# Kernel optimization log

Hardware: AMD Instinct MI355X
Metric: run time of the kernel (lower is better)

Reference implementation:

```python
import jax, jax.numpy as jnp
import numpy as np

INPUT_DIM = 1024
HIDDEN_DIM = 1024


def setup_inputs() -> dict:
    key = jax.random.key(0)
    ks = jax.random.split(key, 7)
    s = 1.0 / np.sqrt(INPUT_DIM)
    x = jax.random.normal(ks[0], (4, 2048, INPUT_DIM), dtype=jnp.float32)
    Wq = jax.random.uniform(ks[1], (INPUT_DIM, HIDDEN_DIM), minval=-s, maxval=s, dtype=jnp.float32)
    bq = jax.random.uniform(ks[2], (HIDDEN_DIM,), minval=-s, maxval=s, dtype=jnp.float32)
    Wk = jax.random.uniform(ks[3], (INPUT_DIM, HIDDEN_DIM), minval=-s, maxval=s, dtype=jnp.float32)
    bk = jax.random.uniform(ks[4], (HIDDEN_DIM,), minval=-s, maxval=s, dtype=jnp.float32)
    Wv = jax.random.uniform(ks[5], (INPUT_DIM, HIDDEN_DIM), minval=-s, maxval=s, dtype=jnp.float32)
    bv = jax.random.uniform(ks[6], (HIDDEN_DIM,), minval=-s, maxval=s, dtype=jnp.float32)
    return {"x": x, "Wq": Wq, "bq": bq, "Wk": Wk, "bk": bk, "Wv": Wv, "bv": bv}


def reference(x, Wq, bq, Wk, bk, Wv, bv):
    # Q, K, V: [B, S, H]
    Q = jnp.einsum('bsd,dh->bsh', x, Wq) + bq
    K = jnp.einsum('bsd,dh->bsh', x, Wk) + bk
    V = jnp.einsum('bsd,dh->bsh', x, Wv) + bv
    scale = 1.0 / jnp.sqrt(jnp.array(Q.shape[-1], dtype=Q.dtype))
    scores = jnp.einsum('bqh,bkh->bqk', Q, K) * scale  # [B, S, S]
    attn = jax.nn.softmax(scores, axis=-1)
    return jnp.einsum('bqk,bkh->bqh', attn, V)
```

## Files before the change

kernel.cpp:

```cpp
#include <hip/hip_runtime.h>
#include <hip/hip_bf16.h>
#include <stdint.h>

typedef unsigned short u16;
typedef __attribute__((ext_vector_type(8))) short short8;
typedef __attribute__((ext_vector_type(4))) float floatx4;

#define DIM 1024

__device__ inline u16 f2bf(float f) {
  union { float f; uint32_t u; } v; v.f = f;
  uint32_t r = v.u + 0x7fffu + ((v.u >> 16) & 1u);
  return (u16)(r >> 16);
}

__device__ inline uint32_t f2bf2(float lo, float hi) {
  __hip_bfloat162 h = __float22bfloat162_rn(float2{lo, hi});
  union { __hip_bfloat162 h; uint32_t u; } v; v.h = h;
  return v.u;
}

__device__ inline void gload_lds16(const u16* g, u16* l) {
  __builtin_amdgcn_global_load_lds((const __attribute__((address_space(1))) uint32_t*)g,
                                   (__attribute__((address_space(3))) uint32_t*)l,
                                   16, 0, 0);
}

#define LGKM0 asm volatile("s_waitcnt lgkmcnt(0)" ::: "memory")
#define VMW(n) asm volatile("s_waitcnt vmcnt(" #n ")" ::: "memory")
#define BAR() do { asm volatile("" ::: "memory"); __builtin_amdgcn_s_barrier(); asm volatile("" ::: "memory"); } while (0)
#define PRIO1 __builtin_amdgcn_s_setprio(1)
#define PRIO0 __builtin_amdgcn_s_setprio(0)

__global__ __launch_bounds__(256) void prep(const float* __restrict__ x,
                                            const float* __restrict__ Wq,
                                            const float* __restrict__ Wk,
                                            const float* __restrict__ Wv,
                                            const float* __restrict__ bq,
                                            const float* __restrict__ bk,
                                            const float* __restrict__ bv,
                                            u16* __restrict__ Xb,
                                            u16* __restrict__ Wt,
                                            float* __restrict__ bias,
                                            float* __restrict__ lsum) {
  __shared__ u16 tile[32][33];
  const int bx = blockIdx.x;
  if (bx < 8192) {
    size_t i = ((size_t)bx * 256 + threadIdx.x) * 4;
    float4 v = *(const float4*)(x + i);
    uint2 o;
    o.x = f2bf2(v.x, v.y);
    o.y = f2bf2(v.z, v.w);
    *(uint2*)(Xb + i) = o;
    if (bx < 8) {
      float4 z = {0.f, 0.f, 0.f, 0.f};
      *(float4*)(lsum + (size_t)bx * 1024 + threadIdx.x * 4) = z;
    }
    return;
  }
  const int t = bx - 8192;
  const int tz = t >> 10;
  const int bxx = t & 31;
  const int byy = (t >> 5) & 31;
  const float* W = (tz == 0) ? Wq : (tz == 1) ? Wk : Wv;
  u16* o = Wt + (size_t)tz * (1u << 20);
  if (bxx == 0 && byy == 0) {
    const float* bsrc = (tz == 0) ? bq : (tz == 1) ? bk : bv;
    float4 b4 = *(const float4*)(bsrc + threadIdx.x * 4);
    *(float4*)(bias + tz * 1024 + threadIdx.x * 4) = b4;
  }
  int c0 = bxx * 32, r0 = byy * 32;
  int tx = threadIdx.x & 31, ty = threadIdx.x >> 5;
#pragma unroll
  for (int p = 0; p < 4; ++p)
    tile[p * 8 + ty][tx] = f2bf(W[(size_t)(r0 + p * 8 + ty) * DIM + c0 + tx]);
  __syncthreads();
#pragma unroll
  for (int p = 0; p < 4; ++p)
    o[(size_t)(c0 + p * 8 + ty) * DIM + r0 + tx] = tile[tx][p * 8 + ty];
}

__device__ __forceinline__ void gemm1024_8ph(const u16* __restrict__ Ab,
                                             const u16* __restrict__ Bb,
                                             u16* __restrict__ lds,
                                             floatx4 (&acc)[8][4]) {
  constexpr int K = 1024;
  constexpr int BUF = 32768;
  const int tid = threadIdx.x;
  const int lane = tid & 63;
  const int w = tid >> 6;
  const int wm = (w >> 2) * 128;
  const int wn = (w & 3) * 64;
  const int fr = lane & 15;
  const int sl0 = (((lane >> 4)    ) ^ (fr & 7)) * 8;
  const int sl1 = (((lane >> 4) | 4) ^ (fr & 7)) * 8;
  const int rA = (wm + fr) * 64;
  const int rB = 16384 + (wn + fr) * 64;
  const int srow = tid >> 3;
  const int kc = ((tid & 7) ^ (srow & 7)) * 8;
  const u16* ga = Ab + (size_t)srow * K + kc;
  const u16* gb = Bb + (size_t)srow * K + kc;
  u16* const ld0 = lds + w * 512;

  short8 Aq[4][2], Bp[2][2][2];

#define STG_A(B_, TT, h) { u16* d_ = ld0 + (B_) * BUF + (h) * 8192;               \
    const u16* s_ = ga + (size_t)((h) * 128) * K + (TT) * 64;                     \
    gload_lds16(s_, d_); gload_lds16(s_ + (size_t)64 * K, d_ + 4096); }
#define STG_B(B_, TT, h) { u16* d_ = ld0 + (B_) * BUF + 16384 + (h) * 8192;       \
    const u16* s_ = gb + (size_t)((h) * 128) * K + (TT) * 64;                     \
    gload_lds16(s_, d_); gload_lds16(s_ + (size_t)64 * K, d_ + 4096); }
#define RD_A(B_, q) { const u16* p_ = lds + (B_) * BUF + rA + (q) * 4096;         \
    _Pragma("unroll") for (int m_ = 0; m_ < 4; ++m_) {                            \
      Aq[m_][0] = *(const short8*)(p_ + m_ * 1024 + sl0);                         \
      Aq[m_][1] = *(const short8*)(p_ + m_ * 1024 + sl1); } }
#define RD_B(B_, p) { const u16* q_ = lds + (B_) * BUF + rB + (p) * 2048;         \
    _Pragma("unroll") for (int n_ = 0; n_ < 2; ++n_) {                            \
      Bp[p][n_][0] = *(const short8*)(q_ + n_ * 1024 + sl0);                      \
      Bp[p][n_][1] = *(const short8*)(q_ + n_ * 1024 + sl1); } }
#define MM(q, p)                                                                  \
    _Pragma("unroll") for (int m_ = 0; m_ < 4; ++m_)                              \
    _Pragma("unroll") for (int n_ = 0; n_ < 2; ++n_)                              \
    _Pragma("unroll") for (int s_ = 0; s_ < 2; ++s_)                              \
      acc[(q) * 4 + m_][(p) * 2 + n_] = __builtin_amdgcn_mfma_f32_16x16x32_bf16(  \
          Aq[m_][s_], Bp[p][n_][s_], acc[(q) * 4 + m_][(p) * 2 + n_], 0, 0, 0);

  STG_A(0, 0, 0); STG_A(0, 0, 1); STG_B(0, 0, 0); STG_B(0, 0, 1);
  STG_B(1, 1, 0); STG_B(1, 1, 1);
  VMW(4);
  BAR();

  for (int j = 0; j < 8; ++j) {
    const int T = 2 * j;
    const bool nl = (j < 7);
    RD_A(0, 0); RD_B(0, 0);
    STG_A(1, T + 1, 0);
    BAR(); LGKM0;
    PRIO1; MM(0, 0); PRIO0;
    BAR();
    RD_B(0, 1);
    STG_A(1, T + 1, 1);
    BAR(); LGKM0;
    PRIO1; MM(0, 1); PRIO0;
    BAR();
    RD_A(0, 1);
    if (nl) STG_B(0, T + 2, 0);
    BAR(); LGKM0;
    PRIO1; MM(1, 0); PRIO0;
    BAR();
    if (nl) STG_B(0, T + 2, 1);
    BAR(); LGKM0;
    PRIO1; MM(1, 1); PRIO0;
    if (nl) { VMW(4); } else { VMW(0); }
    BAR();
    RD_A(1, 0); RD_B(1, 0);
    if (nl) STG_A(0, T + 2, 0);
    BAR(); LGKM0;
    PRIO1; MM(0, 0); PRIO0;
    BAR();
    RD_B(1, 1);
    if (nl) STG_A(0, T + 2, 1);
    BAR(); LGKM0;
    PRIO1; MM(0, 1); PRIO0;
    BAR();
    RD_A(1, 1);
    if (nl) STG_B(1, T + 3, 0);
    BAR(); LGKM0;
    PRIO1; MM(1, 0); PRIO0;
    BAR();
    if (nl) STG_B(1, T + 3, 1);
    BAR(); LGKM0;
    PRIO1; MM(1, 1); PRIO0;
    if (nl) { VMW(4); } else { VMW(0); }
    BAR();
  }
#undef STG_A
#undef STG_B
#undef RD_A
#undef RD_B
#undef MM
}

__global__ __launch_bounds__(512, 2)
void qk_proj(const u16* __restrict__ Xb, const u16* __restrict__ Wt,
             u16* __restrict__ Q, const float* __restrict__ bias) {
  __shared__ __align__(16) u16 lds[65536];
  const int x = blockIdx.x;
  const int c = x & 7, j = x >> 3;
  const int mt = c * 4 + (j & 3);
  const int nt = j >> 2;
  const u16* Ab = Xb + (size_t)mt * 262144;
  const u16* Bb = Wt + (size_t)nt * 262144;
  floatx4 acc[8][4] = {};
  gemm1024_8ph(Ab, Bb, lds, acc);

  const int lane = threadIdx.x & 63;
  const int w = threadIdx.x >> 6;
  const int wm = (w >> 2) * 128, wn = (w & 3) * 64;
  const int er = (lane >> 4) * 4, ec = lane & 15;
  const int r0 = mt * 256 + wm;
  const int z = nt >> 2;
  const int c0 = (nt & 3) * 256 + wn;
  u16* C = Q + (size_t)z * (8u << 20);
  const float* bz = bias + z * 1024;
  const float zs = (z == 0) ? 0.03125f : 1.0f;
#pragma unroll
  for (int mi = 0; mi < 8; ++mi)
#pragma unroll
    for (int ni = 0; ni < 4; ++ni) {
      const int col = c0 + ni * 16 + ec;
      const float bb = bz[col];
      const int row = r0 + mi * 16 + er;
      const uint32_t p0 = f2bf2((acc[mi][ni][0] + bb) * zs, (acc[mi][ni][1] + bb) * zs);
      const uint32_t p1 = f2bf2((acc[mi][ni][2] + bb) * zs, (acc[mi][ni][3] + bb) * zs);
      C[(size_t)(row + 0) * 1024 + col] = (u16)p0;
      C[(size_t)(row + 1) * 1024 + col] = (u16)(p0 >> 16);
      C[(size_t)(row + 2) * 1024 + col] = (u16)p1;
      C[(size_t)(row + 3) * 1024 + col] = (u16)(p1 >> 16);
    }
}

__global__ __launch_bounds__(512, 2)
void vt_score(const u16* __restrict__ Xb, const u16* __restrict__ Wt,
              const u16* __restrict__ Q, u16* __restrict__ Vt,
              u16* __restrict__ P, float* __restrict__ lsum,
              const float* __restrict__ bias) {
  __shared__ __align__(16) u16 lds[65536];
  const int x = blockIdx.x;
  const u16 *Ab, *Bb;
  int mt, nt, z = 0;
  if (x < 128) {
    mt = x & 3; nt = x >> 2;
    Ab = Wt + (size_t)2 * (1u << 20) + (size_t)mt * 262144;
    Bb = Xb + (size_t)nt * 262144;
  } else {
    const int xs = x - 128;
    z = xs >> 6;
    const int q = xs & 63;
    const int c = q & 7, jj = q >> 3;
    mt = (c & 3) * 2 + (jj & 1);
    nt = (c >> 2) * 4 + (jj >> 1);
    Ab = Q + (size_t)z * 2097152 + (size_t)mt * 262144;
    Bb = Q + 8388608 + (size_t)z * 2097152 + (size_t)nt * 262144;
  }
  floatx4 acc[8][4] = {};
  gemm1024_8ph(Ab, Bb, lds, acc);

  const int lane = threadIdx.x & 63;
  const int w = threadIdx.x >> 6;
  const int wm = (w >> 2) * 128, wn = (w & 3) * 64;
  const int er = (lane >> 4) * 4, ec = lane & 15;
  const int r0 = mt * 256 + wm;
  const int c0 = nt * 256 + wn;

  if (x < 128) {
    const float* bz = bias + 2 * 1024;
#pragma unroll
    for (int mi = 0; mi < 8; ++mi) {
      float bb[4];
#pragma unroll
      for (int r = 0; r < 4; ++r) bb[r] = bz[r0 + mi * 16 + er + r];
#pragma unroll
      for (int ni = 0; ni < 4; ++ni) {
        const int col = c0 + ni * 16 + ec;
        const size_t base = (size_t)(col >> 11) * (1u << 21) + (col & 2047);
        const int row = r0 + mi * 16 + er;
        const uint32_t p0 = f2bf2(acc[mi][ni][0] + bb[0], acc[mi][ni][1] + bb[1]);
        const uint32_t p1 = f2bf2(acc[mi][ni][2] + bb[2], acc[mi][ni][3] + bb[3]);
        Vt[base + (size_t)(row + 0) * 2048] = (u16)p0;
        Vt[base + (size_t)(row + 1) * 2048] = (u16)(p0 >> 16);
        Vt[base + (size_t)(row + 2) * 2048] = (u16)p1;
        Vt[base + (size_t)(row + 3) * 2048] = (u16)(p1 >> 16);
      }
    }
  } else {
    u16* C = P + (size_t)z * (4u << 20);
    float* lz = lsum + z * 2048;
#pragma unroll
    for (int mi = 0; mi < 8; ++mi) {
      float rs[4] = {0.f, 0.f, 0.f, 0.f};
#pragma unroll
      for (int ni = 0; ni < 4; ++ni) {
        const int col = c0 + ni * 16 + ec;
        const int row = r0 + mi * 16 + er;
        float e[4];
#pragma unroll
        for (int r = 0; r < 4; ++r) {
          e[r] = exp2f(acc[mi][ni][r] * 1.44269504088896340736f);
          rs[r] += e[r];
        }
        const uint32_t p0 = f2bf2(e[0], e[1]);
        const uint32_t p1 = f2bf2(e[2], e[3]);
        C[(size_t)(row + 0) * 2048 + col] = (u16)p0;
        C[(size_t)(row + 1) * 2048 + col] = (u16)(p0 >> 16);
        C[(size_t)(row + 2) * 2048 + col] = (u16)p1;
        C[(size_t)(row + 3) * 2048 + col] = (u16)(p1 >> 16);
      }
#pragma unroll
      for (int o = 1; o < 16; o <<= 1)
#pragma unroll
        for (int r = 0; r < 4; ++r) rs[r] += __shfl_xor(rs[r], o);
      if ((lane & 15) == 0) {
#pragma unroll
        for (int r = 0; r < 4; ++r)
          atomicAdd(&lz[r0 + mi * 16 + er + r], rs[r]);
      }
    }
  }
}

__global__ __launch_bounds__(512, 2)
void pv_out(const u16* __restrict__ P, const u16* __restrict__ Vt,
            float* __restrict__ out, const float* __restrict__ lsum) {
  __shared__ __align__(16) u16 lds[49152];
  constexpr int K = 2048;
  constexpr int BUF = 24576;
  const int x = blockIdx.x;
  const int z = x >> 6, q = x & 63;
  const int c = q & 7, jj = q >> 3;
  const int mt = (c >> 1) * 4 + (jj & 3);
  const int nt = (c & 1) * 2 + (jj >> 2);
  const u16* Ab = P + (size_t)z * (4u << 20) + (size_t)mt * 128 * 2048;
  const u16* Bb = Vt + (size_t)z * (2u << 20) + (size_t)nt * 256 * 2048;

  const int tid = threadIdx.x;
  const int lane = tid & 63;
  const int w = tid >> 6;
  const int wm = (w >> 2) * 64;
  const int wn = (w & 3) * 64;
  const int fr = lane & 15;
  const int sl0 = (((lane >> 4)    ) ^ (fr & 7)) * 8;
  const int sl1 = (((lane >> 4) | 4) ^ (fr & 7)) * 8;
  const int rA = (wm + fr) * 64;
  const int rB = 8192 + (wn + fr) * 64;
  const int srow = tid >> 3;
  const int kc = ((tid & 7) ^ (srow & 7)) * 8;
  const u16* ga = Ab + (size_t)srow * K + kc;
  const u16* gb = Bb + (size_t)srow * K + kc;
  u16* const ld0 = lds + w * 512;

  short8 Aq[4][2], Bp[2][2][2];
  floatx4 acc[4][4] = {};

#define PSTG_A(B_, TT) { u16* d_ = ld0 + (B_) * BUF;                              \
    const u16* s_ = ga + (size_t)(TT) * 64;                                       \
    gload_lds16(s_, d_); gload_lds16(s_ + (size_t)64 * K, d_ + 4096); }
#define PSTG_B(B_, TT, h) { u16* d_ = ld0 + (B_) * BUF + 8192 + (h) * 8192;       \
    const u16* s_ = gb + (size_t)((h) * 128) * K + (TT) * 64;                     \
    gload_lds16(s_, d_); gload_lds16(s_ + (size_t)64 * K, d_ + 4096); }
#define PRD_A(B_) { const u16* p_ = lds + (B_) * BUF + rA;                        \
    _Pragma("unroll") for (int m_ = 0; m_ < 4; ++m_) {                            \
      Aq[m_][0] = *(const short8*)(p_ + m_ * 1024 + sl0);                         \
      Aq[m_][1] = *(const short8*)(p_ + m_ * 1024 + sl1); } }
#define PRD_B(B_, p) { const u16* q_ = lds + (B_) * BUF + rB + (p) * 2048;        \
    _Pragma("unroll") for (int n_ = 0; n_ < 2; ++n_) {                            \
      Bp[p][n_][0] = *(const short8*)(q_ + n_ * 1024 + sl0);                      \
      Bp[p][n_][1] = *(const short8*)(q_ + n_ * 1024 + sl1); } }
#define PMM(p)                                                                    \
    _Pragma("unroll") for (int m_ = 0; m_ < 4; ++m_)                              \
    _Pragma("unroll") for (int n_ = 0; n_ < 2; ++n_)                              \
    _Pragma("unroll") for (int s_ = 0; s_ < 2; ++s_)                              \
      acc[m_][(p) * 2 + n_] = __builtin_amdgcn_mfma_f32_16x16x32_bf16(            \
          Aq[m_][s_], Bp[p][n_][s_], acc[m_][(p) * 2 + n_], 0, 0, 0);

  PSTG_A(0, 0); PSTG_B(0, 0, 0); PSTG_B(0, 0, 1); PSTG_A(1, 1);
  VMW(2);
  BAR();

  for (int j = 0; j < 16; ++j) {
    const int T = 2 * j;
    const bool nl = (j < 15);
    PRD_A(0); PRD_B(0, 0);
    PSTG_B(1, T + 1, 0); PSTG_B(1, T + 1, 1);
    BAR(); LGKM0;
    PRIO1; PMM(0); PRIO0;
    BAR();
    PRD_B(0, 1);
    if (nl) PSTG_A(0, T + 2);
    BAR(); LGKM0;
    PRIO1; PMM(1); PRIO0;
    if (nl) { VMW(2); } else { VMW(0); }
    BAR();
    PRD_A(1); PRD_B(1, 0);
    if (nl) { PSTG_B(0, T + 2, 0); PSTG_B(0, T + 2, 1); }
    BAR(); LGKM0;
    PRIO1; PMM(0); PRIO0;
    BAR();
    PRD_B(1, 1);
    if (nl) PSTG_A(1, T + 3);
    BAR(); LGKM0;
    PRIO1; PMM(1); PRIO0;
    if (nl) { VMW(2); } else { VMW(0); }
    BAR();
  }
#undef PSTG_A
#undef PSTG_B
#undef PRD_A
#undef PRD_B
#undef PMM

  const int er = (lane >> 4) * 4, ec = lane & 15;
  const int r0 = mt * 128 + wm;
  const int c0 = nt * 256 + wn;
  float* C = out + (size_t)z * (2048 * 1024);
  const float* lz = lsum + z * 2048;
#pragma unroll
  for (int mi = 0; mi < 4; ++mi) {
    float inv[4];
#pragma unroll
    for (int r = 0; r < 4; ++r) inv[r] = 1.0f / lz[r0 + mi * 16 + er + r];
#pragma unroll
    for (int ni = 0; ni < 4; ++ni) {
      const int col = c0 + ni * 16 + ec;
#pragma unroll
      for (int r = 0; r < 4; ++r)
        C[(size_t)(r0 + mi * 16 + er + r) * 1024 + col] = acc[mi][ni][r] * inv[r];
    }
  }
}

extern "C" void kernel_launch(void* const* d_in, const int* in_sizes, int n_in,
                              void* d_out, int out_size, void* d_ws, size_t ws_size,
                              hipStream_t stream) {
  const float* x  = (const float*)d_in[0];
  const float* Wq = (const float*)d_in[1];
  const float* bq = (const float*)d_in[2];
  const float* Wk = (const float*)d_in[3];
  const float* bk = (const float*)d_in[4];
  const float* Wv = (const float*)d_in[5];
  const float* bv = (const float*)d_in[6];
  float* out = (float*)d_out;

  char* ws = (char*)d_ws;
  const size_t MB = 1ull << 20;
  u16* Q    = (u16*)(ws + 0 * MB);
  u16* Vt   = (u16*)(ws + 48 * MB);
  u16* Xb   = (u16*)(ws + 64 * MB);
  u16* Wt   = (u16*)(ws + 80 * MB);
  float* bias = (float*)(ws + 86 * MB);
  float* lsum = (float*)(ws + 87 * MB);
  u16* P    = (u16*)(ws + 88 * MB);
  (void)ws_size; (void)in_sizes; (void)n_in; (void)out_size;

  prep<<<11264, 256, 0, stream>>>(x, Wq, Wk, Wv, bq, bk, bv, Xb, Wt, bias, lsum);
  qk_proj<<<256, 512, 0, stream>>>(Xb, Wt, Q, bias);
  vt_score<<<384, 512, 0, stream>>>(Xb, Wt, Q, Vt, P, lsum, bias);
  pv_out<<<256, 512, 0, stream>>>(P, Vt, out, lsum);
}
```

Measured before the change: 234.3 us.

## Restructure GEMM pipelines to prefetch two k-tiles ahead into the buffer just consumed

```diff
diff --git a/kernel.cpp b/kernel.cpp
--- a/kernel.cpp
+++ b/kernel.cpp
@@ -80,11 +80,12 @@
     o[(size_t)(c0 + p * 8 + ty) * DIM + r0 + tx] = tile[tx][p * 8 + ty];
 }
 
-__device__ __forceinline__ void gemm1024_8ph(const u16* __restrict__ Ab,
+__device__ __forceinline__ void gemm1024_4ph(const u16* __restrict__ Ab,
                                              const u16* __restrict__ Bb,
                                              u16* __restrict__ lds,
                                              floatx4 (&acc)[8][4]) {
   constexpr int K = 1024;
+  constexpr int NT = 16;
   constexpr int BUF = 32768;
   const int tid = threadIdx.x;
   const int lane = tid & 63;
@@ -125,60 +126,49 @@
       acc[(q) * 4 + m_][(p) * 2 + n_] = __builtin_amdgcn_mfma_f32_16x16x32_bf16(  \
           Aq[m_][s_], Bp[p][n_][s_], acc[(q) * 4 + m_][(p) * 2 + n_], 0, 0, 0);
 
+#define HALF_ITER(U)                                                              \
+  {                                                                               \
+    const int u_ = (U) & 1;                                                       \
+    const bool st_ = (U) + 2 < NT;                                                \
+                                                                          \
+    RD_B(u_, 0); RD_B(u_, 1); RD_A(u_, 0);                                        \
+    BAR(); LGKM0;                                                                 \
+    PRIO1; MM(0, 0); PRIO0;                                                       \
+    BAR();                                                                        \
+                                                                          \
+    if (st_) STG_B(u_, (U) + 2, 0);                                               \
+    BAR(); LGKM0;                                                                 \
+    PRIO1; MM(0, 1); PRIO0;                                                       \
+    BAR();                                                                        \
+                                                                          \
+    RD_A(u_, 1);                                                                  \
+    if (st_) STG_B(u_, (U) + 2, 1);                                               \
+    BAR(); LGKM0;                                                                 \
+    PRIO1; MM(1, 0); PRIO0;                                                       \
+    BAR();                                                                        \
+                                                                          \
+    if (st_) { STG_A(u_, (U) + 2, 0); STG_A(u_, (U) + 2, 1); }                    \
+    BAR(); LGKM0;                                                                 \
+    PRIO1; MM(1, 1); PRIO0;                                                       \
+    if (st_) { VMW(8); } else { VMW(0); }                                         \
+    BAR();                                                                        \
+  }
+
   STG_A(0, 0, 0); STG_A(0, 0, 1); STG_B(0, 0, 0); STG_B(0, 0, 1);
-  STG_B(1, 1, 0); STG_B(1, 1, 1);
-  VMW(4);
+  STG_A(1, 1, 0); STG_A(1, 1, 1); STG_B(1, 1, 0); STG_B(1, 1, 1);
+  VMW(8);
   BAR();
 
-  for (int j = 0; j < 8; ++j) {
-    const int T = 2 * j;
-    const bool nl = (j < 7);
-    RD_A(0, 0); RD_B(0, 0);
-    STG_A(1, T + 1, 0);
-    BAR(); LGKM0;
-    PRIO1; MM(0, 0); PRIO0;
-    BAR();
-    RD_B(0, 1);
-    STG_A(1, T + 1, 1);
-    BAR(); LGKM0;
-    PRIO1; MM(0, 1); PRIO0;
-    BAR();
-    RD_A(0, 1);
-    if (nl) STG_B(0, T + 2, 0);
-    BAR(); LGKM0;
-    PRIO1; MM(1, 0); PRIO0;
-    BAR();
-    if (nl) STG_B(0, T + 2, 1);
-    BAR(); LGKM0;
-    PRIO1; MM(1, 1); PRIO0;
-    if (nl) { VMW(4); } else { VMW(0); }
-    BAR();
-    RD_A(1, 0); RD_B(1, 0);
-    if (nl) STG_A(0, T + 2, 0);
-    BAR(); LGKM0;
-    PRIO1; MM(0, 0); PRIO0;
-    BAR();
-    RD_B(1, 1);
-    if (nl) STG_A(0, T + 2, 1);
-    BAR(); LGKM0;
-    PRIO1; MM(0, 1); PRIO0;
-    BAR();
-    RD_A(1, 1);
-    if (nl) STG_B(1, T + 3, 0);
-    BAR(); LGKM0;
-    PRIO1; MM(1, 0); PRIO0;
-    BAR();
-    if (nl) STG_B(1, T + 3, 1);
-    BAR(); LGKM0;
-    PRIO1; MM(1, 1); PRIO0;
-    if (nl) { VMW(4); } else { VMW(0); }
-    BAR();
+  for (int j = 0; j < NT / 2; ++j) {
+    HALF_ITER(2 * j);
+    HALF_ITER(2 * j + 1);
   }
 #undef STG_A
 #undef STG_B
 #undef RD_A
 #undef RD_B
 #undef MM
+#undef HALF_ITER
 }
 
 __global__ __launch_bounds__(512, 2)
@@ -192,7 +182,7 @@
   const u16* Ab = Xb + (size_t)mt * 262144;
   const u16* Bb = Wt + (size_t)nt * 262144;
   floatx4 acc[8][4] = {};
-  gemm1024_8ph(Ab, Bb, lds, acc);
+  gemm1024_4ph(Ab, Bb, lds, acc);
 
   const int lane = threadIdx.x & 63;
   const int w = threadIdx.x >> 6;
@@ -244,7 +234,7 @@
     Bb = Q + 8388608 + (size_t)z * 2097152 + (size_t)nt * 262144;
   }
   floatx4 acc[8][4] = {};
-  gemm1024_8ph(Ab, Bb, lds, acc);
+  gemm1024_4ph(Ab, Bb, lds, acc);
 
   const int lane = threadIdx.x & 63;
   const int w = threadIdx.x >> 6;
@@ -314,6 +304,7 @@
             float* __restrict__ out, const float* __restrict__ lsum) {
   __shared__ __align__(16) u16 lds[49152];
   constexpr int K = 2048;
+  constexpr int NT = 32;
   constexpr int BUF = 24576;
   const int x = blockIdx.x;
   const int z = x >> 6, q = x & 63;
@@ -363,41 +354,38 @@
       acc[m_][(p) * 2 + n_] = __builtin_amdgcn_mfma_f32_16x16x32_bf16(            \
           Aq[m_][s_], Bp[p][n_][s_], acc[m_][(p) * 2 + n_], 0, 0, 0);
 
-  PSTG_A(0, 0); PSTG_B(0, 0, 0); PSTG_B(0, 0, 1); PSTG_A(1, 1);
-  VMW(2);
+#define PHALF(U)                                                                  \
+  {                                                                               \
+    const int u_ = (U) & 1;                                                       \
+    const bool st_ = (U) + 2 < NT;                                                \
+                                                                          \
+    PRD_B(u_, 0); PRD_B(u_, 1); PRD_A(u_);                                        \
+    BAR(); LGKM0;                                                                 \
+    PRIO1; PMM(0); PRIO0;                                                         \
+    BAR();                                                                        \
+                                                                          \
+    if (st_) { PSTG_A(u_, (U) + 2); PSTG_B(u_, (U) + 2, 0); PSTG_B(u_, (U) + 2, 1); } \
+    BAR(); LGKM0;                                                                 \
+    PRIO1; PMM(1); PRIO0;                                                         \
+    if (st_) { VMW(6); } else { VMW(0); }                                         \
+    BAR();                                                                        \
+  }
+
+  PSTG_A(0, 0); PSTG_B(0, 0, 0); PSTG_B(0, 0, 1);
+  PSTG_A(1, 1); PSTG_B(1, 1, 0); PSTG_B(1, 1, 1);
+  VMW(6);
   BAR();
 
-  for (int j = 0; j < 16; ++j) {
-    const int T = 2 * j;
-    const bool nl = (j < 15);
-    PRD_A(0); PRD_B(0, 0);
-    PSTG_B(1, T + 1, 0); PSTG_B(1, T + 1, 1);
-    BAR(); LGKM0;
-    PRIO1; PMM(0); PRIO0;
-    BAR();
-    PRD_B(0, 1);
-    if (nl) PSTG_A(0, T + 2);
-    BAR(); LGKM0;
-    PRIO1; PMM(1); PRIO0;
-    if (nl) { VMW(2); } else { VMW(0); }
-    BAR();
-    PRD_A(1); PRD_B(1, 0);
-    if (nl) { PSTG_B(0, T + 2, 0); PSTG_B(0, T + 2, 1); }
-    BAR(); LGKM0;
-    PRIO1; PMM(0); PRIO0;
-    BAR();
-    PRD_B(1, 1);
-    if (nl) PSTG_A(1, T + 3);
-    BAR(); LGKM0;
-    PRIO1; PMM(1); PRIO0;
-    if (nl) { VMW(2); } else { VMW(0); }
-    BAR();
+  for (int j = 0; j < NT / 2; ++j) {
+    PHALF(2 * j);
+    PHALF(2 * j + 1);
   }
 #undef PSTG_A
 #undef PSTG_B
 #undef PRD_A
 #undef PRD_B
 #undef PMM
+#undef PHALF
 
   const int er = (lane >> 4) * 4, ec = lane & 15;
   const int r0 = mt * 128 + wm;
```

Measured after the change: 237.4 us. Within noise of the previous version (+1.3%).
